# Kernel tuning notes

Measured on AMD Instinct MI355X. Metric: run time of the kernel, lower is better.

The kernel has to match this reference:

```python
import jax, jax.numpy as jnp
import numpy as np
import math

N = 100000        # nodes
E = 3200000       # directed edges (avg degree 32)
F_IN = 256        # in_features
H = 128           # hidden dim (all hidden_dims equal)
L = 4             # number of GCNConvII layers = len(hidden_dims)-1
LAMDA = 0.5
ALPHA = 0.1


def setup_inputs() -> dict:
    key = jax.random.key(0)
    k_x, k_e, k_fw, k_fb, k_w = jax.random.split(key, 5)
    x = jax.random.normal(k_x, (N, F_IN), dtype=jnp.float32)
    edge_index = jax.random.randint(k_e, (2, E), 0, N, dtype=jnp.int32)
    # fc_in: nn.Linear(F_IN, H) default init U(-1/sqrt(F_IN), 1/sqrt(F_IN))
    s_in = 1.0 / math.sqrt(F_IN)
    fc_w = jax.random.uniform(k_fw, (F_IN, H), jnp.float32, -s_in, s_in)
    fc_b = jax.random.uniform(k_fb, (H,), jnp.float32, -s_in, s_in)
    # GCNConvII weight init: U(-1/sqrt(out_channels), 1/sqrt(out_channels))
    s = 1.0 / math.sqrt(H)
    Ws = jax.random.uniform(k_w, (L, H, H), jnp.float32, -s, s)
    return {"x": x, "fc_w": fc_w, "fc_b": fc_b, "Ws": Ws, "edge_index": edge_index}


def reference(x, fc_w, fc_b, Ws, edge_index):
    row = edge_index[0]  # destination nodes (rows of adj)
    col = edge_index[1]  # source nodes (cols of adj)
    # add_self_loops + symmetric normalization: D^{-1/2} (A + I) D^{-1/2}
    deg = jax.ops.segment_sum(jnp.ones((E,), x.dtype), row, num_segments=N) + 1.0
    dinv = jax.lax.rsqrt(deg)
    norm_e = dinv[row] * dinv[col]        # [E] edge weights
    norm_self = 1.0 / deg                 # [N] self-loop weights

    h0 = x @ fc_w + fc_b                  # [N, H]
    h = h0
    for l in range(1, L + 1):
        theta = math.log(LAMDA / l + 1.0)
        # hi = spmm(norm_adj, h): gather source feats, weight, scatter-add to dst
        msgs = h[col] * norm_e[:, None]   # [E, H]
        hi = jax.ops.segment_sum(msgs, row, num_segments=N) + norm_self[:, None] * h
        support = (1.0 - ALPHA) * hi + ALPHA * h0
        out = theta * (support @ Ws[l - 1]) + (1.0 - theta) * support
        h = jax.nn.relu(out) if l < L else out  # no relu on final layer
    return h
```

## Files before the change

kernel.cpp:

```cpp
#include <hip/hip_runtime.h>
#include <math.h>

#define NF 128
#define FIN 256

typedef unsigned short u16;
typedef unsigned int   u32;

__device__ __forceinline__ float bf2f(u16 u) {
    union { u32 i; float f; } v; v.i = ((u32)u) << 16; return v.f;
}
__device__ __forceinline__ u16 f2bf(float f) {
    union { float f; u32 i; } v; v.f = f;
    u32 r = (v.i + 0x7fffu + ((v.i >> 16) & 1u)) >> 16;
    return (u16)r;
}


__global__ void k_deg(const int* __restrict__ row, int* __restrict__ cnt, int E) {
    int e = blockIdx.x * 256 + threadIdx.x;
    if (e < E) atomicAdd(&cnt[row[e]], 1);
}

__global__ __launch_bounds__(1024) void k_scan1(const int* __restrict__ cnt,
                                                int* __restrict__ incl,
                                                int* __restrict__ part, int n) {
    __shared__ int sm[1024];
    const int t = threadIdx.x;
    const int base = blockIdx.x * 1024;
    int v = (base + t < n) ? cnt[base + t] : 0;
    sm[t] = v;
    __syncthreads();
    for (int off = 1; off < 1024; off <<= 1) {
        int u = (t >= off) ? sm[t - off] : 0;
        __syncthreads();
        sm[t] += u;
        __syncthreads();
    }
    if (base + t < n) incl[base + t] = sm[t];
    if (t == 1023) part[blockIdx.x] = sm[1023];
}

__global__ void k_scan2(int* part, int np) {
    __shared__ int sm[128];
    const int t = threadIdx.x;
    int v = (t < np) ? part[t] : 0;
    sm[t] = v;
    __syncthreads();
    for (int off = 1; off < 128; off <<= 1) {
        int u = (t >= off) ? sm[t - off] : 0;
        __syncthreads();
        sm[t] += u;
        __syncthreads();
    }
    if (t < np) part[t] = sm[t] - v;
}

__global__ void k_rowptr(const int* __restrict__ cnt, const int* __restrict__ incl,
                         const int* __restrict__ part, int* __restrict__ rowp,
                         int* __restrict__ curs, float* __restrict__ dinv,
                         float* __restrict__ nself, int n) {
    int i = blockIdx.x * 256 + threadIdx.x;
    if (i >= n) return;
    int start = incl[i] - cnt[i] + part[i >> 10];
    rowp[i] = start;
    curs[i] = start;
    float deg = (float)cnt[i] + 1.0f;
    dinv[i]  = rsqrtf(deg);
    nself[i] = 1.0f / deg;
}

__global__ void k_fill(const int* __restrict__ row, const int* __restrict__ col,
                       const float* __restrict__ dinv, int* __restrict__ curs,
                       int2* __restrict__ meta, int E) {
    int e = blockIdx.x * 256 + threadIdx.x;
    if (e >= E) return;
    int r = row[e], c = col[e];
    int p = atomicAdd(&curs[r], 1);
    float w = dinv[r] * dinv[c];
    meta[p] = make_int2(c, __float_as_int(w));
}


__global__ __launch_bounds__(256) void k_spmm(const u16* __restrict__ tbl,
                                              const u16* __restrict__ h0b,
                                              const int* __restrict__ rowp,
                                              const int* __restrict__ endp,
                                              const int2* __restrict__ meta,
                                              const float* __restrict__ nself,
                                              float* __restrict__ S, int n) {
    const int node = blockIdx.x * 4 + (threadIdx.x >> 6);
    if (node >= n) return;
    const int f2 = (threadIdx.x & 63) << 1;
    const size_t rb = (size_t)node * NF + f2;

    u32 us = *(const u32*)(tbl + rb);
    const float ns = nself[node];
    float ax = ns * bf2f((u16)us);
    float ay = ns * bf2f((u16)(us >> 16));

    int p = rowp[node];
    const int e = endp[node];

    while (p + 8 <= e) {
        int2 m[8];
        #pragma unroll
        for (int i = 0; i < 8; i++) m[i] = meta[p + i];
        u32 u[8];
        #pragma unroll
        for (int i = 0; i < 8; i++)
            u[i] = *(const u32*)(tbl + (size_t)m[i].x * NF + f2);
        #pragma unroll
        for (int i = 0; i < 8; i++) {
            float w = __int_as_float(m[i].y);
            ax = fmaf(w, bf2f((u16)u[i]),         ax);
            ay = fmaf(w, bf2f((u16)(u[i] >> 16)), ay);
        }
        p += 8;
    }
    while (p < e) {
        int2 mm = meta[p++];
        float w = __int_as_float(mm.y);
        u32 u = *(const u32*)(tbl + (size_t)mm.x * NF + f2);
        ax = fmaf(w, bf2f((u16)u),         ax);
        ay = fmaf(w, bf2f((u16)(u >> 16)), ay);
    }

    u32 u0 = *(const u32*)(h0b + rb);
    float2 o;
    o.x = 0.9f * ax + 0.1f * bf2f((u16)u0);
    o.y = 0.9f * ay + 0.1f * bf2f((u16)(u0 >> 16));
    *(float2*)(S + rb) = o;
}


template<int K, int MODE>
__global__ __launch_bounds__(256) void k_gemm(const float* __restrict__ A,
                                              const float* __restrict__ B,
                                              const float* __restrict__ X,
                                              float* __restrict__ Cf,
                                              u16* __restrict__ Cb,
                                              int nrows, float theta) {
    __shared__ float As[64 * 32];
    __shared__ float Bs[32 * NF];
    const int tid = threadIdx.x;
    const int tr = tid >> 5;
    const int tc = tid & 31;
    const int rowbase = blockIdx.x * 64;

    float4 acc[8];
    #pragma unroll
    for (int i = 0; i < 8; i++) acc[i] = make_float4(0.f, 0.f, 0.f, 0.f);

    for (int k0 = 0; k0 < K; k0 += 32) {
        #pragma unroll
        for (int p = 0; p < 2; p++) {
            int i  = tid + p * 256;
            int r  = i >> 3;
            int kq = (i & 7) << 2;
            int gr = rowbase + r;
            float4 v = make_float4(0.f, 0.f, 0.f, 0.f);
            if (gr < nrows) v = *(const float4*)(A + (size_t)gr * K + k0 + kq);
            *(float4*)(As + r * 32 + kq) = v;
        }
        #pragma unroll
        for (int p = 0; p < 4; p++) {
            int i  = tid + p * 256;
            int br = i >> 5;
            int bc = (i & 31) << 2;
            *(float4*)(Bs + br * NF + bc) = *(const float4*)(B + (size_t)(k0 + br) * NF + bc);
        }
        __syncthreads();
        #pragma unroll
        for (int kk4 = 0; kk4 < 8; kk4++) {
            float4 av[8];
            #pragma unroll
            for (int i = 0; i < 8; i++)
                av[i] = *(const float4*)(As + (tr * 8 + i) * 32 + kk4 * 4);
            #pragma unroll
            for (int j = 0; j < 4; j++) {
                float4 b = *(const float4*)(Bs + (kk4 * 4 + j) * NF + (tc << 2));
                #pragma unroll
                for (int i = 0; i < 8; i++) {
                    float a = (j == 0) ? av[i].x : (j == 1) ? av[i].y : (j == 2) ? av[i].z : av[i].w;
                    acc[i].x = fmaf(a, b.x, acc[i].x);
                    acc[i].y = fmaf(a, b.y, acc[i].y);
                    acc[i].z = fmaf(a, b.z, acc[i].z);
                    acc[i].w = fmaf(a, b.w, acc[i].w);
                }
            }
        }
        __syncthreads();
    }

    const float om = 1.0f - theta;
    #pragma unroll
    for (int i = 0; i < 8; i++) {
        int gr = rowbase + tr * 8 + i;
        if (gr >= nrows) continue;
        float4 o = acc[i];
        if (MODE == 0) {
            float4 bb = *(const float4*)(X + (tc << 2));
            o.x += bb.x; o.y += bb.y; o.z += bb.z; o.w += bb.w;
        } else {
            float4 s = *(const float4*)(X + (size_t)gr * NF + (tc << 2));
            o.x = theta * o.x + om * s.x;
            o.y = theta * o.y + om * s.y;
            o.z = theta * o.z + om * s.z;
            o.w = theta * o.w + om * s.w;
            if (MODE == 1) {
                o.x = fmaxf(o.x, 0.f); o.y = fmaxf(o.y, 0.f);
                o.z = fmaxf(o.z, 0.f); o.w = fmaxf(o.w, 0.f);
            }
        }
        if (MODE == 2) {
            *(float4*)(Cf + (size_t)gr * NF + (tc << 2)) = o;
        } else {
            u32 u0 = (u32)f2bf(o.x) | ((u32)f2bf(o.y) << 16);
            u32 u1 = (u32)f2bf(o.z) | ((u32)f2bf(o.w) << 16);
            uint2 pk; pk.x = u0; pk.y = u1;
            *(uint2*)(Cb + (size_t)gr * NF + (tc << 2)) = pk;
        }
    }
}


extern "C" void kernel_launch(void* const* d_in, const int* in_sizes, int n_in,
                              void* d_out, int out_size, void* d_ws, size_t ws_size,
                              hipStream_t stream) {
    const float* x   = (const float*)d_in[0];
    const float* fcw = (const float*)d_in[1];
    const float* fcb = (const float*)d_in[2];
    const float* Ws  = (const float*)d_in[3];
    const int*   ei  = (const int*)d_in[4];
    const int N = in_sizes[0] / FIN;
    const int E = in_sizes[4] / 2;
    const int* row = ei;
    const int* col = ei + E;
    float* out = (float*)d_out;

    char* base = (char*)d_ws;
    size_t off = 0;
    auto alloc = [&](size_t b) -> char* {
        char* p = base + off;
        off += (b + 255) & ~(size_t)255;
        return p;
    };
    u16*   h0b   = (u16*)alloc((size_t)N * NF * sizeof(u16));
    u16*   hb    = (u16*)alloc((size_t)N * NF * sizeof(u16));
    float* S     = (float*)alloc((size_t)N * NF * sizeof(float));
    int2*  meta  = (int2*)alloc((size_t)E * sizeof(int2));
    int*   cnt   = (int*)alloc((size_t)N * sizeof(int));
    int*   incl  = (int*)alloc((size_t)N * sizeof(int));
    int*   rowp  = (int*)alloc((size_t)N * sizeof(int));
    int*   curs  = (int*)alloc((size_t)N * sizeof(int));
    float* dinv  = (float*)alloc((size_t)N * sizeof(float));
    float* nself = (float*)alloc((size_t)N * sizeof(float));
    int*   part  = (int*)alloc(1024);
    if (off > ws_size) return;

    hipMemsetAsync(cnt, 0, (size_t)N * sizeof(int), stream);
    const int eb = (E + 255) / 256;
    k_deg<<<eb, 256, 0, stream>>>(row, cnt, E);
    const int nch = (N + 1023) / 1024;
    k_scan1<<<nch, 1024, 0, stream>>>(cnt, incl, part, N);
    k_scan2<<<1, 128, 0, stream>>>(part, nch);
    k_rowptr<<<(N + 255) / 256, 256, 0, stream>>>(cnt, incl, part, rowp, curs, dinv, nself, N);
    k_fill<<<eb, 256, 0, stream>>>(row, col, dinv, curs, meta, E);

    const int gb = (N + 63) / 64;
    k_gemm<FIN, 0><<<gb, 256, 0, stream>>>(x, fcw, fcb, nullptr, h0b, N, 0.f);

    const float thetas[4] = { logf(1.5f), logf(1.25f), logf(0.5f / 3.f + 1.f), logf(1.125f) };
    const u16* tbl = h0b;
    for (int l = 1; l <= 4; l++) {
        k_spmm<<<(N + 3) / 4, 256, 0, stream>>>(tbl, h0b, rowp, curs, meta, nself, S, N);
        const float* W = Ws + (size_t)(l - 1) * NF * NF;
        if (l < 4) {
            k_gemm<NF, 1><<<gb, 256, 0, stream>>>(S, W, S, nullptr, hb, N, thetas[l - 1]);
            tbl = hb;
        } else {
            k_gemm<NF, 2><<<gb, 256, 0, stream>>>(S, W, S, out, nullptr, N, thetas[3]);
        }
    }
}
```

Before: 1.210 ms.

## Prescale features by D^-1/2, fold theta into weights, use bf16 MFMA GEMMs

Stores node features pre-multiplied by D^-1/2 so the SpMM drops per-edge weights and reads only 4-byte column indices instead of 8-byte (col, weight) metadata. Folds theta*W + (1-theta)*I into a single bf16 weight matrix, pre-swizzled into MFMA fragment order. Replaces the fp32 FMA tiled GEMMs with bf16 MFMA 16x16x32 kernels, and writes the intermediate S in bf16 instead of fp32. The cost is extra bf16 rounding, including on the inputs, the folded identity term and S, which may reduce accuracy.

Measured after the change: 1.126 ms. -6.9%, faster.

```diff
diff --git a/kernel.cpp b/kernel.cpp
--- a/kernel.cpp
+++ b/kernel.cpp
@@ -6,6 +6,10 @@
 
 typedef unsigned short u16;
 typedef unsigned int   u32;
+typedef __bf16 bf16x8 __attribute__((ext_vector_type(8)));
+typedef float  f32x4  __attribute__((ext_vector_type(4)));
+
+union ABu { uint4 u; bf16x8 v; u16 s[8]; };
 
 __device__ __forceinline__ float bf2f(u16 u) {
     union { u32 i; float f; } v; v.i = ((u32)u) << 16; return v.f;
@@ -58,168 +62,167 @@
 
 __global__ void k_rowptr(const int* __restrict__ cnt, const int* __restrict__ incl,
                          const int* __restrict__ part, int* __restrict__ rowp,
-                         int* __restrict__ curs, float* __restrict__ dinv,
-                         float* __restrict__ nself, int n) {
+                         int* __restrict__ curs, float2* __restrict__ dnode, int n) {
     int i = blockIdx.x * 256 + threadIdx.x;
     if (i >= n) return;
     int start = incl[i] - cnt[i] + part[i >> 10];
     rowp[i] = start;
     curs[i] = start;
     float deg = (float)cnt[i] + 1.0f;
-    dinv[i]  = rsqrtf(deg);
-    nself[i] = 1.0f / deg;
+    dnode[i] = make_float2(rsqrtf(deg), sqrtf(deg));
 }
 
 __global__ void k_fill(const int* __restrict__ row, const int* __restrict__ col,
-                       const float* __restrict__ dinv, int* __restrict__ curs,
-                       int2* __restrict__ meta, int E) {
+                       int* __restrict__ curs, int* __restrict__ ccol, int E) {
     int e = blockIdx.x * 256 + threadIdx.x;
     if (e >= E) return;
-    int r = row[e], c = col[e];
+    int r = row[e];
     int p = atomicAdd(&curs[r], 1);
-    float w = dinv[r] * dinv[c];
-    meta[p] = make_int2(c, __float_as_int(w));
-}
-
-
-__global__ __launch_bounds__(256) void k_spmm(const u16* __restrict__ tbl,
-                                              const u16* __restrict__ h0b,
+    ccol[p] = col[e];
+}
+
+
+__global__ void k_prepB0(const float* __restrict__ fcw, u16* __restrict__ dst) {
+    int idx = blockIdx.x * 256 + threadIdx.x;
+    int e = idx & 7, l = (idx >> 3) & 63, j = (idx >> 9) & 7, s = idx >> 12;
+    int k = s * 32 + (l >> 4) * 8 + e, n = j * 16 + (l & 15);
+    dst[idx] = f2bf(fcw[k * NF + n]);
+}
+
+__global__ void k_prepBl(const float* __restrict__ Ws, u16* __restrict__ dst, float4 th) {
+    int idx = blockIdx.x * 256 + threadIdx.x;
+    int e = idx & 7, l = (idx >> 3) & 63, j = (idx >> 9) & 7, s = (idx >> 12) & 3, ly = idx >> 14;
+    int k = s * 32 + (l >> 4) * 8 + e, n = j * 16 + (l & 15);
+    float t = (ly == 0) ? th.x : (ly == 1) ? th.y : (ly == 2) ? th.z : th.w;
+    float w = t * Ws[(size_t)ly * NF * NF + k * NF + n] + ((k == n) ? (1.f - t) : 0.f);
+    dst[idx] = f2bf(w);
+}
+
+
+__global__ __launch_bounds__(256) void k_spmm(const u16* __restrict__ tblp,
+                                              const u16* __restrict__ tbl0p,
                                               const int* __restrict__ rowp,
                                               const int* __restrict__ endp,
-                                              const int2* __restrict__ meta,
-                                              const float* __restrict__ nself,
-                                              float* __restrict__ S, int n) {
+                                              const int* __restrict__ ccol,
+                                              const float2* __restrict__ dnode,
+                                              u16* __restrict__ Sb, int n) {
     const int node = blockIdx.x * 4 + (threadIdx.x >> 6);
     if (node >= n) return;
     const int f2 = (threadIdx.x & 63) << 1;
     const size_t rb = (size_t)node * NF + f2;
 
-    u32 us = *(const u32*)(tbl + rb);
-    const float ns = nself[node];
-    float ax = ns * bf2f((u16)us);
-    float ay = ns * bf2f((u16)(us >> 16));
+    u32 us = *(const u32*)(tblp + rb);
+    float ax = bf2f((u16)us), ay = bf2f((u16)(us >> 16));
 
     int p = rowp[node];
     const int e = endp[node];
-
     while (p + 8 <= e) {
-        int2 m[8];
-        #pragma unroll
-        for (int i = 0; i < 8; i++) m[i] = meta[p + i];
+        int c[8];
+        #pragma unroll
+        for (int i = 0; i < 8; i++) c[i] = ccol[p + i];
         u32 u[8];
         #pragma unroll
         for (int i = 0; i < 8; i++)
-            u[i] = *(const u32*)(tbl + (size_t)m[i].x * NF + f2);
+            u[i] = *(const u32*)(tblp + (size_t)c[i] * NF + f2);
         #pragma unroll
         for (int i = 0; i < 8; i++) {
-            float w = __int_as_float(m[i].y);
-            ax = fmaf(w, bf2f((u16)u[i]),         ax);
-            ay = fmaf(w, bf2f((u16)(u[i] >> 16)), ay);
+            ax += bf2f((u16)u[i]);
+            ay += bf2f((u16)(u[i] >> 16));
         }
         p += 8;
     }
     while (p < e) {
-        int2 mm = meta[p++];
-        float w = __int_as_float(mm.y);
-        u32 u = *(const u32*)(tbl + (size_t)mm.x * NF + f2);
-        ax = fmaf(w, bf2f((u16)u),         ax);
-        ay = fmaf(w, bf2f((u16)(u >> 16)), ay);
-    }
-
-    u32 u0 = *(const u32*)(h0b + rb);
-    float2 o;
-    o.x = 0.9f * ax + 0.1f * bf2f((u16)u0);
-    o.y = 0.9f * ay + 0.1f * bf2f((u16)(u0 >> 16));
-    *(float2*)(S + rb) = o;
+        int c = ccol[p++];
+        u32 u = *(const u32*)(tblp + (size_t)c * NF + f2);
+        ax += bf2f((u16)u);
+        ay += bf2f((u16)(u >> 16));
+    }
+
+    const float2 dn = dnode[node];
+    u32 h0u = *(const u32*)(tbl0p + rb);
+    float ox = 0.9f * dn.x * ax + 0.1f * dn.y * bf2f((u16)h0u);
+    float oy = 0.9f * dn.x * ay + 0.1f * dn.y * bf2f((u16)(h0u >> 16));
+    *(u32*)(Sb + rb) = (u32)f2bf(ox) | ((u32)f2bf(oy) << 16);
 }
 
 
 template<int K, int MODE>
-__global__ __launch_bounds__(256) void k_gemm(const float* __restrict__ A,
-                                              const float* __restrict__ B,
-                                              const float* __restrict__ X,
-                                              float* __restrict__ Cf,
-                                              u16* __restrict__ Cb,
-                                              int nrows, float theta) {
-    __shared__ float As[64 * 32];
-    __shared__ float Bs[32 * NF];
+__global__ __launch_bounds__(256) void k_gemmM(const void* __restrict__ Ap,
+                                               const uint4* __restrict__ Bfrag,
+                                               const float* __restrict__ bias,
+                                               const float2* __restrict__ dnode,
+                                               u16* __restrict__ Cb,
+                                               float* __restrict__ Cf,
+                                               int nrows) {
+    constexpr int KS = K / 32;
+    __shared__ u16 Bs[K * NF];
     const int tid = threadIdx.x;
-    const int tr = tid >> 5;
-    const int tc = tid & 31;
-    const int rowbase = blockIdx.x * 64;
-
-    float4 acc[8];
+    constexpr int NV = K * NF / 8;
+    uint4* Bs4 = (uint4*)Bs;
+    for (int i = tid; i < NV; i += 256) Bs4[i] = Bfrag[i];
+    __syncthreads();
+
+    const int lane = tid & 63, wave = tid >> 6;
+    const int m = lane & 15, kg = lane >> 4;
+    const int row = blockIdx.x * 64 + wave * 16 + m;
+    const bool rok = row < nrows;
+
+    ABu af[KS];
+    if (MODE == 0) {
+        const float* A = (const float*)Ap;
+        #pragma unroll
+        for (int s = 0; s < KS; s++) {
+            float4 f0 = {0.f, 0.f, 0.f, 0.f}, f1 = {0.f, 0.f, 0.f, 0.f};
+            if (rok) {
+                f0 = *(const float4*)(A + (size_t)row * K + s * 32 + kg * 8);
+                f1 = *(const float4*)(A + (size_t)row * K + s * 32 + kg * 8 + 4);
+            }
+            af[s].s[0] = f2bf(f0.x); af[s].s[1] = f2bf(f0.y);
+            af[s].s[2] = f2bf(f0.z); af[s].s[3] = f2bf(f0.w);
+            af[s].s[4] = f2bf(f1.x); af[s].s[5] = f2bf(f1.y);
+            af[s].s[6] = f2bf(f1.z); af[s].s[7] = f2bf(f1.w);
+        }
+    } else {
+        const u16* A = (const u16*)Ap;
+        #pragma unroll
+        for (int s = 0; s < KS; s++) {
+            if (rok) af[s].u = *(const uint4*)(A + (size_t)row * K + s * 32 + kg * 8);
+            else     af[s].u = make_uint4(0, 0, 0, 0);
+        }
+    }
+
+    f32x4 acc[8];
     #pragma unroll
-    for (int i = 0; i < 8; i++) acc[i] = make_float4(0.f, 0.f, 0.f, 0.f);
-
-    for (int k0 = 0; k0 < K; k0 += 32) {
-        #pragma unroll
-        for (int p = 0; p < 2; p++) {
-            int i  = tid + p * 256;
-            int r  = i >> 3;
-            int kq = (i & 7) << 2;
-            int gr = rowbase + r;
-            float4 v = make_float4(0.f, 0.f, 0.f, 0.f);
-            if (gr < nrows) v = *(const float4*)(A + (size_t)gr * K + k0 + kq);
-            *(float4*)(As + r * 32 + kq) = v;
-        }
-        #pragma unroll
-        for (int p = 0; p < 4; p++) {
-            int i  = tid + p * 256;
-            int br = i >> 5;
-            int bc = (i & 31) << 2;
-            *(float4*)(Bs + br * NF + bc) = *(const float4*)(B + (size_t)(k0 + br) * NF + bc);
-        }
-        __syncthreads();
-        #pragma unroll
-        for (int kk4 = 0; kk4 < 8; kk4++) {
-            float4 av[8];
+    for (int j = 0; j < 8; j++) acc[j] = (f32x4){0.f, 0.f, 0.f, 0.f};
+
+    #pragma unroll
+    for (int s = 0; s < KS; s++) {
+        #pragma unroll
+        for (int j = 0; j < 8; j++) {
+            ABu b;
+            b.u = *((const uint4*)Bs + (s * 8 + j) * 64 + lane);
+            acc[j] = __builtin_amdgcn_mfma_f32_16x16x32_bf16(af[s].v, b.v, acc[j], 0, 0, 0);
+        }
+    }
+
+    const int orow0 = blockIdx.x * 64 + wave * 16 + kg * 4;
+    #pragma unroll
+    for (int r = 0; r < 4; r++) {
+        const int orow = orow0 + r;
+        if (orow >= nrows) continue;
+        if (MODE == 2) {
             #pragma unroll
-            for (int i = 0; i < 8; i++)
-                av[i] = *(const float4*)(As + (tr * 8 + i) * 32 + kk4 * 4);
+            for (int j = 0; j < 8; j++)
+                Cf[(size_t)orow * NF + j * 16 + m] = acc[j][r];
+        } else {
+            const float dv = dnode[orow].x;
             #pragma unroll
-            for (int j = 0; j < 4; j++) {
-                float4 b = *(const float4*)(Bs + (kk4 * 4 + j) * NF + (tc << 2));
-                #pragma unroll
-                for (int i = 0; i < 8; i++) {
-                    float a = (j == 0) ? av[i].x : (j == 1) ? av[i].y : (j == 2) ? av[i].z : av[i].w;
-                    acc[i].x = fmaf(a, b.x, acc[i].x);
-                    acc[i].y = fmaf(a, b.y, acc[i].y);
-                    acc[i].z = fmaf(a, b.z, acc[i].z);
-                    acc[i].w = fmaf(a, b.w, acc[i].w);
-                }
+            for (int j = 0; j < 8; j++) {
+                float v = acc[j][r];
+                if (MODE == 0) v += bias[j * 16 + m];
+                else           v = fmaxf(v, 0.f);
+                Cb[(size_t)orow * NF + j * 16 + m] = f2bf(dv * v);
             }
-        }
-        __syncthreads();
-    }
-
-    const float om = 1.0f - theta;
-    #pragma unroll
-    for (int i = 0; i < 8; i++) {
-        int gr = rowbase + tr * 8 + i;
-        if (gr >= nrows) continue;
-        float4 o = acc[i];
-        if (MODE == 0) {
-            float4 bb = *(const float4*)(X + (tc << 2));
-            o.x += bb.x; o.y += bb.y; o.z += bb.z; o.w += bb.w;
-        } else {
-            float4 s = *(const float4*)(X + (size_t)gr * NF + (tc << 2));
-            o.x = theta * o.x + om * s.x;
-            o.y = theta * o.y + om * s.y;
-            o.z = theta * o.z + om * s.z;
-            o.w = theta * o.w + om * s.w;
-            if (MODE == 1) {
-                o.x = fmaxf(o.x, 0.f); o.y = fmaxf(o.y, 0.f);
-                o.z = fmaxf(o.z, 0.f); o.w = fmaxf(o.w, 0.f);
-            }
-        }
-        if (MODE == 2) {
-            *(float4*)(Cf + (size_t)gr * NF + (tc << 2)) = o;
-        } else {
-            u32 u0 = (u32)f2bf(o.x) | ((u32)f2bf(o.y) << 16);
-            u32 u1 = (u32)f2bf(o.z) | ((u32)f2bf(o.w) << 16);
-            uint2 pk; pk.x = u0; pk.y = u1;
-            *(uint2*)(Cb + (size_t)gr * NF + (tc << 2)) = pk;
         }
     }
 }
@@ -246,17 +249,18 @@
         off += (b + 255) & ~(size_t)255;
         return p;
     };
-    u16*   h0b   = (u16*)alloc((size_t)N * NF * sizeof(u16));
-    u16*   hb    = (u16*)alloc((size_t)N * NF * sizeof(u16));
-    float* S     = (float*)alloc((size_t)N * NF * sizeof(float));
-    int2*  meta  = (int2*)alloc((size_t)E * sizeof(int2));
-    int*   cnt   = (int*)alloc((size_t)N * sizeof(int));
-    int*   incl  = (int*)alloc((size_t)N * sizeof(int));
-    int*   rowp  = (int*)alloc((size_t)N * sizeof(int));
-    int*   curs  = (int*)alloc((size_t)N * sizeof(int));
-    float* dinv  = (float*)alloc((size_t)N * sizeof(float));
-    float* nself = (float*)alloc((size_t)N * sizeof(float));
-    int*   part  = (int*)alloc(1024);
+    u16*    tbl0p = (u16*)alloc((size_t)N * NF * sizeof(u16));
+    u16*    hb    = (u16*)alloc((size_t)N * NF * sizeof(u16));
+    u16*    Sb    = (u16*)alloc((size_t)N * NF * sizeof(u16));
+    int*    ccol  = (int*)alloc((size_t)E * sizeof(int));
+    u16*    Bf0   = (u16*)alloc(32768 * sizeof(u16));
+    u16*    Bfl   = (u16*)alloc(65536 * sizeof(u16));
+    int*    cnt   = (int*)alloc((size_t)N * sizeof(int));
+    int*    incl  = (int*)alloc((size_t)N * sizeof(int));
+    int*    rowp  = (int*)alloc((size_t)N * sizeof(int));
+    int*    curs  = (int*)alloc((size_t)N * sizeof(int));
+    float2* dnode = (float2*)alloc((size_t)N * sizeof(float2));
+    int*    part  = (int*)alloc(1024);
     if (off > ws_size) return;
 
     hipMemsetAsync(cnt, 0, (size_t)N * sizeof(int), stream);
@@ -265,22 +269,25 @@
     const int nch = (N + 1023) / 1024;
     k_scan1<<<nch, 1024, 0, stream>>>(cnt, incl, part, N);
     k_scan2<<<1, 128, 0, stream>>>(part, nch);
-    k_rowptr<<<(N + 255) / 256, 256, 0, stream>>>(cnt, incl, part, rowp, curs, dinv, nself, N);
-    k_fill<<<eb, 256, 0, stream>>>(row, col, dinv, curs, meta, E);
+    k_rowptr<<<(N + 255) / 256, 256, 0, stream>>>(cnt, incl, part, rowp, curs, dnode, N);
+    k_fill<<<eb, 256, 0, stream>>>(row, col, curs, ccol, E);
+
+    const float4 th4 = make_float4(logf(1.5f), logf(1.25f), logf(7.f / 6.f), logf(1.125f));
+    k_prepB0<<<128, 256, 0, stream>>>(fcw, Bf0);
+    k_prepBl<<<256, 256, 0, stream>>>(Ws, Bfl, th4);
 
     const int gb = (N + 63) / 64;
-    k_gemm<FIN, 0><<<gb, 256, 0, stream>>>(x, fcw, fcb, nullptr, h0b, N, 0.f);
-
-    const float thetas[4] = { logf(1.5f), logf(1.25f), logf(0.5f / 3.f + 1.f), logf(1.125f) };
-    const u16* tbl = h0b;
+    k_gemmM<FIN, 0><<<gb, 256, 0, stream>>>(x, (const uint4*)Bf0, fcb, dnode, tbl0p, nullptr, N);
+
+    const u16* tbl = tbl0p;
     for (int l = 1; l <= 4; l++) {
-        k_spmm<<<(N + 3) / 4, 256, 0, stream>>>(tbl, h0b, rowp, curs, meta, nself, S, N);
-        const float* W = Ws + (size_t)(l - 1) * NF * NF;
+        k_spmm<<<(N + 3) / 4, 256, 0, stream>>>(tbl, tbl0p, rowp, curs, ccol, dnode, Sb, N);
+        const uint4* Bf = (const uint4*)(Bfl + (size_t)(l - 1) * 16384);
         if (l < 4) {
-            k_gemm<NF, 1><<<gb, 256, 0, stream>>>(S, W, S, nullptr, hb, N, thetas[l - 1]);
+            k_gemmM<NF, 1><<<gb, 256, 0, stream>>>(Sb, Bf, nullptr, dnode, hb, nullptr, N);
             tbl = hb;
         } else {
-            k_gemm<NF, 2><<<gb, 256, 0, stream>>>(S, W, S, out, nullptr, N, thetas[3]);
-        }
-    }
-}
+            k_gemmM<NF, 2><<<gb, 256, 0, stream>>>(Sb, Bf, nullptr, nullptr, nullptr, out, N);
+        }
+    }
+}
```
